# Optimization experiments

Measured on AMD Instinct MI355X. Metric: run time of the kernel, lower is better.

## Reference

```python
import jax, jax.numpy as jnp
import numpy as np

B, C, N, K = 2, 128, 10000, 16


def setup_inputs() -> dict:
    key = jax.random.key(0)
    k1, k2, k3, k4 = jax.random.split(key, 4)
    x = jax.random.normal(k1, (B, C, N, 1), dtype=jnp.float32)
    edge_index = jax.random.randint(k2, (2, B, N, K), 0, N, dtype=jnp.int32)
    W = jax.random.normal(k3, (C, C), dtype=jnp.float32) * 0.05  # 1x1 conv C->C, no bias
    a = jax.random.normal(k4, (2 * C,), dtype=jnp.float32) * 0.05  # 1x1 conv 2C->1, no bias
    return {"x": x, "edge_index": edge_index, "W": W, "a": a}


def reference(x, edge_index, W, a):
    # x: [B,C,N,1], edge_index: [2,B,N,K]
    b, c, n, _ = x.shape
    k = edge_index.shape[-1]
    xs = x[..., 0]  # [B,C,N]
    wh = jnp.einsum('oc,bcn->bon', W, xs)  # 1x1 conv W(x): [B,C,N]
    # batched_index_select: gather along node dim -> [B,C,N,K]
    idx_i = edge_index[1].reshape(b, 1, n * k)
    idx_j = edge_index[0].reshape(b, 1, n * k)
    whi = jnp.take_along_axis(wh, idx_i, axis=2).reshape(b, c, n, k)
    whj = jnp.take_along_axis(wh, idx_j, axis=2).reshape(b, c, n, k)
    # a(cat([whi, whj], dim=1)) with a: 2C->1 == a_i . whi + a_j . whj
    e = jnp.einsum('c,bcnk->bnk', a[:c], whi) + jnp.einsum('c,bcnk->bnk', a[c:], whj)
    e = jax.nn.leaky_relu(e, negative_slope=0.2)
    A = jax.nn.softmax(e, axis=-1)  # [B,N,K]; dropout omitted (eval mode)
    h = jnp.einsum('bcnk,bnk->bcn', whj, A)  # mul + sum over K
    return h[..., None]  # [B,C,N,1]
```

## Files before the change

kernel.cpp:

```cpp
#include <hip/hip_runtime.h>


#define BB 2
#define CC 128
#define NN 10000
#define KK 16
#define TNG 32
#define TNA 16
#define LSTR 136

typedef unsigned int uint32;
typedef __attribute__((ext_vector_type(8))) short short8;
typedef __attribute__((ext_vector_type(4))) float floatx4;

__device__ __forceinline__ uint32 bf16pair(float lo, float hi) {
  uint32 ulo = __float_as_uint(lo);
  uint32 uhi = __float_as_uint(hi);
  ulo += 0x7fffu + ((ulo >> 16) & 1u);
  uhi += 0x7fffu + ((uhi >> 16) & 1u);
  return (ulo >> 16) | (uhi & 0xffff0000u);
}

__global__ __launch_bounds__(256) void gat_gemm(
    const float* __restrict__ x,
    const float* __restrict__ W,
    const float* __restrict__ a,
    uint32* __restrict__ wht,
    float* __restrict__ si,
    float* __restrict__ sj) {
  __shared__ unsigned short xs[TNG * LSTR];
  __shared__ float red[2][4][2][16];

  const int b    = blockIdx.y;
  const int n0   = blockIdx.x * TNG;
  const int t    = threadIdx.x;
  const int w    = t >> 6;
  const int lane = t & 63;
  const int col  = lane & 15;
  const int q    = lane >> 4;

  {
    const float* xb = x + (size_t)b * CC * NN;
    uint32* xd = (uint32*)xs;
#pragma unroll
    for (int i = 0; i < 8; ++i) {
      int e = t + i * 256;
      int n = e & 31, cp = e >> 5;
      int c = cp * 2, gn = n0 + n;
      float v0 = 0.f, v1 = 0.f;
      if (gn < NN) { v0 = xb[c * NN + gn]; v1 = xb[(c + 1) * NN + gn]; }
      xd[n * 68 + cp] = bf16pair(v0, v1);
    }
  }

  short8 af[2][4];
#pragma unroll
  for (int ci = 0; ci < 2; ++ci) {
    const float* wr = W + (w * 32 + ci * 16 + col) * CC;
#pragma unroll
    for (int s = 0; s < 4; ++s) {
      float4 f0 = *(const float4*)(wr + s * 32 + q * 8);
      float4 f1 = *(const float4*)(wr + s * 32 + q * 8 + 4);
      union { uint32 u[4]; short8 v; } cv;
      cv.u[0] = bf16pair(f0.x, f0.y);
      cv.u[1] = bf16pair(f0.z, f0.w);
      cv.u[2] = bf16pair(f1.x, f1.y);
      cv.u[3] = bf16pair(f1.z, f1.w);
      af[ci][s] = cv.v;
    }
  }
  __syncthreads();

  floatx4 acc[2][2];
#pragma unroll
  for (int ci = 0; ci < 2; ++ci)
#pragma unroll
    for (int nj = 0; nj < 2; ++nj) acc[ci][nj] = (floatx4){0.f, 0.f, 0.f, 0.f};

#pragma unroll
  for (int s = 0; s < 4; ++s) {
    short8 bf[2];
#pragma unroll
    for (int nj = 0; nj < 2; ++nj)
      bf[nj] = *(const short8*)(xs + (nj * 16 + col) * LSTR + s * 32 + q * 8);
#pragma unroll
    for (int ci = 0; ci < 2; ++ci)
#pragma unroll
      for (int nj = 0; nj < 2; ++nj)
        acc[ci][nj] = __builtin_amdgcn_mfma_f32_16x16x32_bf16(af[ci][s], bf[nj], acc[ci][nj], 0, 0, 0);
  }

  float ar[2][4], aj4[2][4];
#pragma unroll
  for (int ci = 0; ci < 2; ++ci)
#pragma unroll
    for (int r = 0; r < 4; ++r) {
      int ch = w * 32 + ci * 16 + q * 4 + r;
      ar[ci][r]  = a[ch];
      aj4[ci][r] = a[CC + ch];
    }

#pragma unroll
  for (int nj = 0; nj < 2; ++nj) {
    int node = n0 + nj * 16 + col;
    float psi = 0.f, psj = 0.f;
#pragma unroll
    for (int ci = 0; ci < 2; ++ci) {
#pragma unroll
      for (int r = 0; r < 4; ++r) {
        psi = fmaf(ar[ci][r], acc[ci][nj][r], psi);
        psj = fmaf(aj4[ci][r], acc[ci][nj][r], psj);
      }
      if (node < NN) {
        uint2 pk;
        pk.x = bf16pair(acc[ci][nj][0], acc[ci][nj][1]);
        pk.y = bf16pair(acc[ci][nj][2], acc[ci][nj][3]);
        uint2* dst = (uint2*)(wht + ((size_t)(b * NN + node)) * (CC / 2) + w * 16 + ci * 8 + q * 2);
        *dst = pk;
      }
    }
    psi += __shfl_down(psi, 32);
    psi += __shfl_down(psi, 16);
    psj += __shfl_down(psj, 32);
    psj += __shfl_down(psj, 16);
    if (q == 0) { red[0][w][nj][col] = psi; red[1][w][nj][col] = psj; }
  }
  __syncthreads();

  if (t < TNG) {
    int gn = n0 + t;
    if (gn < NN) {
      int nj = t >> 4, cl = t & 15;
      float s1 = 0.f, s2 = 0.f;
#pragma unroll
      for (int ww = 0; ww < 4; ++ww) { s1 += red[0][ww][nj][cl]; s2 += red[1][ww][nj][cl]; }
      si[b * NN + gn] = s1;
      sj[b * NN + gn] = s2;
    }
  }
}

__global__ __launch_bounds__(256) void gat_gather(
    const int* __restrict__ ei,
    const uint32* __restrict__ wht,
    const float* __restrict__ si,
    const float* __restrict__ sj,
    float* __restrict__ out) {
  __shared__ float Am[TNA][KK];
  __shared__ int   jd[TNA][KK];
  __shared__ float outT[CC][TNA + 1];

  const int bk   = blockIdx.x;
  const int xcd  = bk & 7;
  const int b    = xcd >> 2;
  const int slot = (bk >> 3) * 4 + (xcd & 3);
  if (slot >= (NN + TNA - 1) / TNA) return;
  const int n0 = slot * TNA;
  const int t  = threadIdx.x;

  const int* eij = ei + b * NN * KK;
  const int* eii = ei + (BB + b) * NN * KK;
  const float* sib = si + b * NN;
  const float* sjb = sj + b * NN;

  {
    int nn = t >> 4, k = t & 15, gn = n0 + nn;
    float el = 0.f; int jj = 0;
    if (gn < NN) {
      jj = eij[gn * KK + k];
      int ii = eii[gn * KK + k];
      float v = sib[ii] + sjb[jj];
      el = (v > 0.f) ? v : 0.2f * v;
    }
    Am[nn][k] = el;
    jd[nn][k] = jj;
  }
  __syncthreads();

  if (t < TNA) {
    float mx = Am[t][0];
#pragma unroll
    for (int k = 1; k < KK; ++k) mx = fmaxf(mx, Am[t][k]);
    float s = 0.f, ex[KK];
#pragma unroll
    for (int k = 0; k < KK; ++k) { ex[k] = __expf(Am[t][k] - mx); s += ex[k]; }
    float inv = 1.f / s;
#pragma unroll
    for (int k = 0; k < KK; ++k) Am[t][k] = ex[k] * inv;
  }
  __syncthreads();

  const int cp = t & 63;
  const int nw = t >> 6;
  const uint32* whtb = wht + (size_t)b * NN * (CC / 2);
#pragma unroll
  for (int half = 0; half < 2; ++half) {
    int na = nw + half * 4;
    int idx[2][KK]; float wk[2][KK];
#pragma unroll
    for (int p = 0; p < 2; ++p) {
      int nn = na + p * 8;
      const uint4*  jp = (const uint4*)&jd[nn][0];
      const float4* ap = (const float4*)&Am[nn][0];
#pragma unroll
      for (int g = 0; g < 4; ++g) {
        uint4  jv = jp[g];
        float4 av = ap[g];
        idx[p][4 * g + 0] = jv.x; idx[p][4 * g + 1] = jv.y;
        idx[p][4 * g + 2] = jv.z; idx[p][4 * g + 3] = jv.w;
        wk[p][4 * g + 0] = av.x;  wk[p][4 * g + 1] = av.y;
        wk[p][4 * g + 2] = av.z;  wk[p][4 * g + 3] = av.w;
      }
    }
    uint32 v[2][KK];
#pragma unroll
    for (int p = 0; p < 2; ++p)
#pragma unroll
      for (int k = 0; k < KK; ++k)
        v[p][k] = whtb[(size_t)idx[p][k] * (CC / 2) + cp];
#pragma unroll
    for (int p = 0; p < 2; ++p) {
      int nn = na + p * 8;
      float ax = 0.f, ay = 0.f;
#pragma unroll
      for (int k = 0; k < KK; ++k) {
        ax = fmaf(wk[p][k], __uint_as_float(v[p][k] << 16), ax);
        ay = fmaf(wk[p][k], __uint_as_float(v[p][k] & 0xffff0000u), ay);
      }
      outT[2 * cp][nn]     = ax;
      outT[2 * cp + 1][nn] = ay;
    }
  }
  __syncthreads();

  float* outb = out + (size_t)b * CC * NN;
#pragma unroll
  for (int i = 0; i < (CC * TNA) / 256; ++i) {
    int e = t + i * 256;
    int c = e >> 4, nn = e & 15;
    int gn = n0 + nn;
    if (gn < NN) outb[c * NN + gn] = outT[c][nn];
  }
}

extern "C" void kernel_launch(void* const* d_in, const int* in_sizes, int n_in,
                              void* d_out, int out_size, void* d_ws, size_t ws_size,
                              hipStream_t stream) {
  const float* x  = (const float*)d_in[0];
  const int*   ei = (const int*)d_in[1];
  const float* W  = (const float*)d_in[2];
  const float* a  = (const float*)d_in[3];
  float* out = (float*)d_out;

  uint32* wht = (uint32*)d_ws;
  float*  si  = (float*)(wht + (size_t)BB * NN * (CC / 2));
  float*  sj  = si + BB * NN;

  dim3 g1((NN + TNG - 1) / TNG, BB);
  gat_gemm<<<g1, 256, 0, stream>>>(x, W, a, wht, si, sj);
  gat_gather<<<dim3(157 * 8), 256, 0, stream>>>(ei, wht, si, sj, out);
}
```

Measured before the change: 86.57 us.

## Double node tiles in GEMM and gather, compute softmax with wave shuffles

The GEMM tile grows to 64 nodes per block, so each wave reuses its W fragments across four MFMA column tiles, and the gather tile grows to 32 nodes with a grid resized to match. The softmax in the gather kernel no longer runs serially on 16 threads between two barriers. It is now done per 16-lane group with xor shuffles, which removes one __syncthreads and the single-thread loops. The cost is fewer blocks, which lowers parallelism on a small problem, and higher register pressure from the larger accumulator arrays.

```diff
diff --git a/kernel.cpp b/kernel.cpp
--- a/kernel.cpp
+++ b/kernel.cpp
@@ -5,8 +5,8 @@
 #define CC 128
 #define NN 10000
 #define KK 16
-#define TNG 32
-#define TNA 16
+#define TNG 64
+#define TNA 32
 #define LSTR 136
 
 typedef unsigned int uint32;
@@ -29,7 +29,7 @@
     float* __restrict__ si,
     float* __restrict__ sj) {
   __shared__ unsigned short xs[TNG * LSTR];
-  __shared__ float red[2][4][2][16];
+  __shared__ float red[2][4][4][16];
 
   const int b    = blockIdx.y;
   const int n0   = blockIdx.x * TNG;
@@ -43,9 +43,9 @@
     const float* xb = x + (size_t)b * CC * NN;
     uint32* xd = (uint32*)xs;
 #pragma unroll
-    for (int i = 0; i < 8; ++i) {
+    for (int i = 0; i < 16; ++i) {
       int e = t + i * 256;
-      int n = e & 31, cp = e >> 5;
+      int n = e & 63, cp = e >> 6;
       int c = cp * 2, gn = n0 + n;
       float v0 = 0.f, v1 = 0.f;
       if (gn < NN) { v0 = xb[c * NN + gn]; v1 = xb[(c + 1) * NN + gn]; }
@@ -71,22 +71,22 @@
   }
   __syncthreads();
 
-  floatx4 acc[2][2];
+  floatx4 acc[2][4];
 #pragma unroll
   for (int ci = 0; ci < 2; ++ci)
 #pragma unroll
-    for (int nj = 0; nj < 2; ++nj) acc[ci][nj] = (floatx4){0.f, 0.f, 0.f, 0.f};
+    for (int nj = 0; nj < 4; ++nj) acc[ci][nj] = (floatx4){0.f, 0.f, 0.f, 0.f};
 
 #pragma unroll
   for (int s = 0; s < 4; ++s) {
-    short8 bf[2];
-#pragma unroll
-    for (int nj = 0; nj < 2; ++nj)
+    short8 bf[4];
+#pragma unroll
+    for (int nj = 0; nj < 4; ++nj)
       bf[nj] = *(const short8*)(xs + (nj * 16 + col) * LSTR + s * 32 + q * 8);
 #pragma unroll
     for (int ci = 0; ci < 2; ++ci)
 #pragma unroll
-      for (int nj = 0; nj < 2; ++nj)
+      for (int nj = 0; nj < 4; ++nj)
         acc[ci][nj] = __builtin_amdgcn_mfma_f32_16x16x32_bf16(af[ci][s], bf[nj], acc[ci][nj], 0, 0, 0);
   }
 
@@ -101,7 +101,7 @@
     }
 
 #pragma unroll
-  for (int nj = 0; nj < 2; ++nj) {
+  for (int nj = 0; nj < 4; ++nj) {
     int node = n0 + nj * 16 + col;
     float psi = 0.f, psj = 0.f;
 #pragma unroll
@@ -163,30 +163,23 @@
   const float* sib = si + b * NN;
   const float* sjb = sj + b * NN;
 
-  {
-    int nn = t >> 4, k = t & 15, gn = n0 + nn;
-    float el = 0.f; int jj = 0;
-    if (gn < NN) {
-      jj = eij[gn * KK + k];
-      int ii = eii[gn * KK + k];
-      float v = sib[ii] + sjb[jj];
-      el = (v > 0.f) ? v : 0.2f * v;
-    }
-    Am[nn][k] = el;
+#pragma unroll
+  for (int r = 0; r < 2; ++r) {
+    int e = t + r * 256;
+    int nn = e >> 4, k = e & 15, gn = n0 + nn;
+    int jj = 0, ii = 0;
+    if (gn < NN) { jj = eij[gn * KK + k]; ii = eii[gn * KK + k]; }
+    float v = sib[ii] + sjb[jj];
+    float el = (v > 0.f) ? v : 0.2f * v;
+    float mx = el;
+#pragma unroll
+    for (int d = 1; d < KK; d <<= 1) mx = fmaxf(mx, __shfl_xor(mx, d));
+    float ex = __expf(el - mx);
+    float s = ex;
+#pragma unroll
+    for (int d = 1; d < KK; d <<= 1) s += __shfl_xor(s, d);
+    Am[nn][k] = ex / s;
     jd[nn][k] = jj;
-  }
-  __syncthreads();
-
-  if (t < TNA) {
-    float mx = Am[t][0];
-#pragma unroll
-    for (int k = 1; k < KK; ++k) mx = fmaxf(mx, Am[t][k]);
-    float s = 0.f, ex[KK];
-#pragma unroll
-    for (int k = 0; k < KK; ++k) { ex[k] = __expf(Am[t][k] - mx); s += ex[k]; }
-    float inv = 1.f / s;
-#pragma unroll
-    for (int k = 0; k < KK; ++k) Am[t][k] = ex[k] * inv;
   }
   __syncthreads();
 
@@ -194,12 +187,12 @@
   const int nw = t >> 6;
   const uint32* whtb = wht + (size_t)b * NN * (CC / 2);
 #pragma unroll
-  for (int half = 0; half < 2; ++half) {
-    int na = nw + half * 4;
+  for (int pr = 0; pr < 4; ++pr) {
+    int na = nw * 8 + pr * 2;
     int idx[2][KK]; float wk[2][KK];
 #pragma unroll
     for (int p = 0; p < 2; ++p) {
-      int nn = na + p * 8;
+      int nn = na + p;
       const uint4*  jp = (const uint4*)&jd[nn][0];
       const float4* ap = (const float4*)&Am[nn][0];
 #pragma unroll
@@ -220,7 +213,7 @@
         v[p][k] = whtb[(size_t)idx[p][k] * (CC / 2) + cp];
 #pragma unroll
     for (int p = 0; p < 2; ++p) {
-      int nn = na + p * 8;
+      int nn = na + p;
       float ax = 0.f, ay = 0.f;
 #pragma unroll
       for (int k = 0; k < KK; ++k) {
@@ -237,7 +230,7 @@
 #pragma unroll
   for (int i = 0; i < (CC * TNA) / 256; ++i) {
     int e = t + i * 256;
-    int c = e >> 4, nn = e & 15;
+    int c = e >> 5, nn = e & 31;
     int gn = n0 + nn;
     if (gn < NN) outb[c * NN + gn] = outT[c][nn];
   }
@@ -258,5 +251,5 @@
 
   dim3 g1((NN + TNG - 1) / TNG, BB);
   gat_gemm<<<g1, 256, 0, stream>>>(x, W, a, wht, si, sj);
-  gat_gather<<<dim3(157 * 8), 256, 0, stream>>>(ei, wht, si, sj, out);
-}
+  gat_gather<<<dim3(79 * 8), 256, 0, stream>>>(ei, wht, si, sj, out);
+}
```

Result: slower. 90.89 us (+5.0%).
